# Kernel optimization log

Measured on AMD Instinct MI355X. Metric: run time of the kernel, lower is better.

Reference implementation:

```python
import jax, jax.numpy as jnp
import numpy as np

HID = 64        # HID_DIM of seq2seq encoder
NL = 2          # N_LAYERS
D = HID * NL    # dim_hidden = 128
TYPES = 16      # node op types; Input=0, Const=1
MAX_ET = 32     # max edge_type id
NUM_ROUNDS = 2


def _gru_cell(x, h, Wih, Whh, bih, bhh):
    # torch GRU gate ordering: r, z, n
    gi = x @ Wih.T + bih
    gh = h @ Whh.T + bhh
    ir, iz, inn = jnp.split(gi, 3, axis=-1)
    hr, hz, hn = jnp.split(gh, 3, axis=-1)
    r = jax.nn.sigmoid(ir + hr)
    z = jax.nn.sigmoid(iz + hz)
    n = jnp.tanh(inn + r * hn)
    return (1.0 - z) * n + z * h


def _posenc(n, d):
    pos = jnp.arange(n, dtype=jnp.float32)[:, None]
    i = jnp.arange(d // 2, dtype=jnp.float32)[None, :]
    inv = jnp.exp(-jnp.log(10000.0) * (2.0 * i / d))
    pe = jnp.zeros((n, d), jnp.float32)
    pe = pe.at[:, 0::2].set(jnp.sin(pos * inv))
    pe = pe.at[:, 1::2].set(jnp.cos(pos * inv))
    return pe


def _forward(x, edge_index, edge_type, sim_res, seq_len,
             enc_Wih0, enc_Whh0, enc_bih0, enc_bhh0,
             enc_Wih1, enc_Whh1, enc_bih1, enc_bhh1,
             Wq, Wk, Wv, op_emb, mlp_W1, mlp_b1, mlp_W2, mlp_b2,
             gru_Wih, gru_Whh, gru_bih, gru_bhh):
    N = x.shape[0]
    # --- seq2seq encode (2-layer GRU over time), computed for all nodes then masked ---
    xs = jnp.swapaxes(sim_res[:, :seq_len, :], 0, 1)  # [T, N, W]
    h0 = jnp.zeros((N, HID), sim_res.dtype)
    h1 = jnp.zeros((N, HID), sim_res.dtype)

    def step(carry, xt):
        h0, h1 = carry
        h0 = _gru_cell(xt, h0, enc_Wih0, enc_Whh0, enc_bih0, enc_bhh0)
        h1 = _gru_cell(h0, h1, enc_Wih1, enc_Whh1, enc_bih1, enc_bhh1)
        return (h0, h1), None

    (h0, h1), _ = jax.lax.scan(step, (h0, h1), xs)
    enc = jnp.concatenate([h0, h1], axis=-1)  # [N, D] = permute(1,0,2).flatten(1)
    mask = (x[:, 0] == 1) | (x[:, 1] == 1)    # Input | Const nodes
    node_emb = jnp.where(mask[:, None], enc, 0.0)

    src, dst = edge_index[0], edge_index[1]
    edge_op = jnp.argmax(x[dst], axis=1)       # [E]
    pe = _posenc(MAX_ET, D)
    edge_feat = pe[edge_type] + op_emb[edge_op]  # [E, D]
    scale = 1.0 / jnp.sqrt(jnp.float32(D))

    for _ in range(NUM_ROUNDS):
        kf = node_emb[src] + edge_feat         # [E, D]
        q = node_emb[dst] @ Wq.T
        k = kf @ Wk.T
        v = kf @ Wv.T
        score = jnp.sum(q * k, axis=-1) * scale  # [E]
        m = jax.ops.segment_max(score, dst, num_segments=N)
        ex = jnp.exp(score - m[dst])
        den = jax.ops.segment_sum(ex, dst, num_segments=N)
        alpha = ex / (den[dst] + 1e-9)
        aggr = jax.ops.segment_sum(alpha[:, None] * v, dst, num_segments=N)  # [N, D]
        aggr = jax.nn.relu(aggr @ mlp_W1.T + mlp_b1) @ mlp_W2.T + mlp_b2
        node_emb = _gru_cell(aggr, node_emb, gru_Wih, gru_Whh, gru_bih, gru_bhh)
    return node_emb


def setup_inputs() -> dict:
    key = jax.random.key(0)
    ks = jax.random.split(key, 24)
    N, E, T, W = 20000, 320000, 32, 32
    s = 0.05

    def g(k, shape):
        return jax.random.normal(k, shape, dtype=jnp.float32) * s

    node_type = jax.random.randint(ks[0], (N,), 0, TYPES)
    x = jax.nn.one_hot(node_type, TYPES, dtype=jnp.float32)
    edge_index = jax.random.randint(ks[1], (2, E), 0, N)
    edge_type = jax.random.randint(ks[2], (E,), 0, MAX_ET)
    sim_res = jax.random.uniform(ks[3], (N, T, W), dtype=jnp.float32)
    return {
        "x": x, "edge_index": edge_index, "edge_type": edge_type,
        "sim_res": sim_res, "seq_len": 32,
        "enc_Wih0": g(ks[4], (3 * HID, W)), "enc_Whh0": g(ks[5], (3 * HID, HID)),
        "enc_bih0": g(ks[6], (3 * HID,)), "enc_bhh0": g(ks[7], (3 * HID,)),
        "enc_Wih1": g(ks[8], (3 * HID, HID)), "enc_Whh1": g(ks[9], (3 * HID, HID)),
        "enc_bih1": g(ks[10], (3 * HID,)), "enc_bhh1": g(ks[11], (3 * HID,)),
        "Wq": g(ks[12], (D, D)), "Wk": g(ks[13], (D, D)), "Wv": g(ks[14], (D, D)),
        "op_emb": g(ks[15], (TYPES, D)),
        "mlp_W1": g(ks[16], (D, D)), "mlp_b1": g(ks[17], (D,)),
        "mlp_W2": g(ks[18], (D, D)), "mlp_b2": g(ks[19], (D,)),
        "gru_Wih": g(ks[20], (3 * D, D)), "gru_Whh": g(ks[21], (3 * D, D)),
        "gru_bih": g(ks[22], (3 * D,)), "gru_bhh": g(ks[23], (3 * D,)),
    }


def reference(x, edge_index, edge_type, sim_res, seq_len,
              enc_Wih0, enc_Whh0, enc_bih0, enc_bhh0,
              enc_Wih1, enc_Whh1, enc_bih1, enc_bhh1,
              Wq, Wk, Wv, op_emb, mlp_W1, mlp_b1, mlp_W2, mlp_b2,
              gru_Wih, gru_Whh, gru_bih, gru_bhh):
    return _forward(x, edge_index, edge_type, sim_res, seq_len,
                    enc_Wih0, enc_Whh0, enc_bih0, enc_bhh0,
                    enc_Wih1, enc_Whh1, enc_bih1, enc_bhh1,
                    Wq, Wk, Wv, op_emb, mlp_W1, mlp_b1, mlp_W2, mlp_b2,
                    gru_Wih, gru_Whh, gru_bih, gru_bhh)
```

## Files before the change

### kernel.cpp

```cpp
#include <hip/hip_runtime.h>

typedef unsigned int uint;
typedef unsigned short ushort;

typedef __attribute__((ext_vector_type(8))) short bf8;
typedef __attribute__((ext_vector_type(4))) float f32x4;
typedef _Float16 half_t;
typedef __attribute__((ext_vector_type(8))) half_t h8;

__device__ __forceinline__ ushort f2bf(float f){
  uint u = __builtin_bit_cast(uint, f);
  u = u + 0x7FFFu + ((u >> 16) & 1u);
  return (ushort)(u >> 16);
}
__device__ __forceinline__ float bfl(uint u){ return __builtin_bit_cast(float, u << 16); }
__device__ __forceinline__ float bfh(uint u){ return __builtin_bit_cast(float, u & 0xFFFF0000u); }
__device__ __forceinline__ uint pkhalf(float a, float b){
  ushort lo = __builtin_bit_cast(ushort, (half_t)a);
  ushort hi = __builtin_bit_cast(ushort, (half_t)b);
  return (uint)lo | ((uint)hi << 16);
}
__device__ __forceinline__ float sigmoidf_(float x){ return 1.0f/(1.0f + __expf(-x)); }
__device__ __forceinline__ float tanhf_(float x){
  x = fminf(15.0f, fmaxf(-15.0f, x));
  float t = __expf(-2.0f*x);
  return (1.0f - t)/(1.0f + t);
}
__device__ __forceinline__ f32x4 mfma_f16(h8 a, h8 b, f32x4 c){
  return __builtin_amdgcn_mfma_f32_16x16x32_f16(a, b, c, 0, 0, 0);
}
__device__ __forceinline__ f32x4 mfma_bf(bf8 a, bf8 b, f32x4 c){
  return __builtin_amdgcn_mfma_f32_16x16x32_bf16(a, b, c, 0, 0, 0);
}
__device__ __forceinline__ h8 ldw8(const float* p){
  f32x4 a = *(const f32x4*)p, b = *(const f32x4*)(p+4);
  h8 v;
  #pragma unroll
  for (int j=0;j<4;j++){ v[j] = (half_t)a[j]; v[4+j] = (half_t)b[j]; }
  return v;
}

__global__ __launch_bounds__(256) void k_prep(const float* __restrict__ x,
    const int* __restrict__ dst,
    int* __restrict__ typ, int* __restrict__ mlist, int* __restrict__ cnt,
    int* __restrict__ deg, float* __restrict__ Hf, ushort* __restrict__ Hb,
    int N, int E){
  int i = blockIdx.x*256 + threadIdx.x;
  int total = gridDim.x*256;
  if (i < N){
    const float* xr = x + (size_t)i*16;
    int t = 0;
    #pragma unroll
    for (int j=0;j<16;j++) if (xr[j] > 0.5f) t = j;
    typ[i] = t;
    if (t < 2){
      int p = atomicAdd(cnt, 1);
      mlist[p] = i;
    }
  }
  if (i < E) atomicAdd(&deg[dst[i]], 1);
  f32x4 z4 = (f32x4)0.0f;
  for (int j = i; j < N*32; j += total) ((f32x4*)Hf)[j] = z4;
  uint2 z2; z2.x = 0u; z2.y = 0u;
  for (int j = i; j < N*32; j += total) ((uint2*)Hb)[j] = z2;
}

__global__ __launch_bounds__(256) void k_cvt(
    const float* wq, const float* wk, const float* wv,
    const float* w1, const float* w2, const float* wih, const float* whh,
    const float* __restrict__ op_emb,
    ushort* oqkv, ushort* o1, ushort* o2, ushort* oih, ushort* ohh,
    ushort* __restrict__ EF){
  int i = blockIdx.x*256 + threadIdx.x;
  int stride = gridDim.x*256;
  for (int j=i; j<16384; j+=stride){
    oqkv[j]       = f2bf(wq[j]);
    oqkv[16384+j] = f2bf(wk[j]);
    oqkv[32768+j] = f2bf(wv[j]);
    o1[j] = f2bf(w1[j]);
    o2[j] = f2bf(w2[j]);
  }
  for (int j=i; j<49152; j+=stride){ oih[j]=f2bf(wih[j]); ohh[j]=f2bf(whh[j]); }
  for (int idx=i; idx<512*128; idx+=stride){
    int r = idx >> 7, d = idx & 127;
    int et = r >> 4, op = r & 15;
    int j = d >> 1;
    float inv = __expf(-0.1439115683f * (float)j);
    float ang = (float)et * inv;
    float v = (d & 1) ? __cosf(ang) : __sinf(ang);
    EF[idx] = f2bf(v + op_emb[op*128 + d]);
  }
}

template<int RELU, int HASBIAS>
__global__ __launch_bounds__(256) void k_gemm(
    const ushort* __restrict__ A, const ushort* __restrict__ B,
    const float* __restrict__ bias, ushort* __restrict__ C, int M, int N){
  int lane = threadIdx.x & 63, wv = threadIdx.x >> 6;
  int tM = blockIdx.x*64 + (wv>>1)*32;
  int tN = blockIdx.y*64 + (wv&1)*32;
  int r16 = lane & 15, kg = (lane>>4)*8;
  f32x4 acc[2][2];
  #pragma unroll
  for (int i=0;i<2;i++)
    #pragma unroll
    for (int j=0;j<2;j++) acc[i][j] = (f32x4)0.0f;
  #pragma unroll
  for (int k0=0;k0<128;k0+=32){
    bf8 a[2], b[2];
    #pragma unroll
    for (int i=0;i<2;i++){
      int row = tM + i*16 + r16; if (row > M-1) row = M-1;
      a[i] = *(const bf8*)(A + (size_t)row*128 + k0 + kg);
    }
    #pragma unroll
    for (int j=0;j<2;j++){
      int col = tN + j*16 + r16;
      b[j] = *(const bf8*)(B + (size_t)col*128 + k0 + kg);
    }
    #pragma unroll
    for (int i=0;i<2;i++)
      #pragma unroll
      for (int j=0;j<2;j++)
        acc[i][j] = __builtin_amdgcn_mfma_f32_16x16x32_bf16(a[i], b[j], acc[i][j], 0, 0, 0);
  }
  #pragma unroll
  for (int i=0;i<2;i++)
    #pragma unroll
    for (int j=0;j<2;j++){
      int col = tN + j*16 + r16;
      float bs = HASBIAS ? bias[col] : 0.0f;
      #pragma unroll
      for (int q=0;q<4;q++){
        int row = tM + i*16 + (lane>>4)*4 + q;
        if (row < M){
          float v = acc[i][j][q] + bs;
          if (RELU) v = fmaxf(v, 0.0f);
          C[(size_t)row*N + col] = f2bf(v);
        }
      }
    }
}

__global__ __launch_bounds__(512, 1) void k_enc4(
    const float* __restrict__ sim_res, const int* __restrict__ seqlen,
    const float* __restrict__ Wih0, const float* __restrict__ Whh0,
    const float* __restrict__ bih0, const float* __restrict__ bhh0,
    const float* __restrict__ Wih1, const float* __restrict__ Whh1,
    const float* __restrict__ bih1, const float* __restrict__ bhh1,
    const int* __restrict__ mlist, const int* __restrict__ cntp,
    float* __restrict__ Hf, ushort* __restrict__ Hb){
  int C = *cntp;
  int base = blockIdx.x * 16;
  if (C == 0 || base >= C) return;
  int tid = threadIdx.x;
  int w = tid >> 6, l = tid & 63;
  int node = l & 15, hi = l >> 4;
  int grp = w >> 2;
  int ws  = w & 3;

  __shared__ int nod[16];
  __shared__ __align__(16) float  Xs[16*32*32];
  __shared__ __align__(16) ushort H0h[2][16*64], H1h[2][16*64];

  if (tid < 16){
    int idx = base + tid;
    nod[tid] = mlist[idx < C ? idx : C-1];
  }
  for (int i = tid; i < 16*64; i += 512){
    H0h[0][i] = 0; H0h[1][i] = 0; H1h[0][i] = 0; H1h[1][i] = 0;
  }
  __syncthreads();

  for (int m = tid; m < 4096; m += 512){
    int nm = m >> 8, tt = (m >> 3) & 31, c = m & 7;
    int cs = c ^ (nm & 7);
    f32x4 v = *(const f32x4*)(sim_res + (size_t)nod[nm]*1024 + tt*32 + cs*4);
    *(f32x4*)(Xs + m*4) = v;
  }

  int rr = 16*ws + node;
  h8 zf;
  #pragma unroll
  for (int j=0;j<8;j++) zf[j] = (half_t)0.f;
  h8 Ai_r[2] = {zf, zf}, Ai_z[2] = {zf, zf}, Ai_n[2] = {zf, zf};
  h8 Ah_r[2], Ah_z[2], Ah_n[2];
  if (grp == 0){
    Ai_r[0] = ldw8(Wih0 + (size_t)rr*32        + hi*8);
    Ai_z[0] = ldw8(Wih0 + (size_t)(64+rr)*32   + hi*8);
    Ai_n[0] = ldw8(Wih0 + (size_t)(128+rr)*32  + hi*8);
    #pragma unroll
    for (int s=0;s<2;s++){
      Ah_r[s] = ldw8(Whh0 + (size_t)rr*64       + s*32 + hi*8);
      Ah_z[s] = ldw8(Whh0 + (size_t)(64+rr)*64  + s*32 + hi*8);
      Ah_n[s] = ldw8(Whh0 + (size_t)(128+rr)*64 + s*32 + hi*8);
    }
  } else {
    #pragma unroll
    for (int s=0;s<2;s++){
      Ai_r[s] = ldw8(Wih1 + (size_t)rr*64       + s*32 + hi*8);
      Ai_z[s] = ldw8(Wih1 + (size_t)(64+rr)*64  + s*32 + hi*8);
      Ai_n[s] = ldw8(Wih1 + (size_t)(128+rr)*64 + s*32 + hi*8);
      Ah_r[s] = ldw8(Whh1 + (size_t)rr*64       + s*32 + hi*8);
      Ah_z[s] = ldw8(Whh1 + (size_t)(64+rr)*64  + s*32 + hi*8);
      Ah_n[s] = ldw8(Whh1 + (size_t)(128+rr)*64 + s*32 + hi*8);
    }
  }
  const float* bi = grp ? bih1 : bih0;
  const float* bh = grp ? bhh1 : bhh0;
  float br[4], bz[4], bni[4], bnh[4];
  #pragma unroll
  for (int q=0;q<4;q++){
    int row = 16*ws + hi*4 + q;
    br[q]  = bi[row]      + bh[row];
    bz[q]  = bi[64+row]   + bh[64+row];
    bni[q] = bi[128+row];
    bnh[q] = bh[128+row];
  }

  int T = *seqlen; if (T > 32) T = 32; if (T < 0) T = 0;
  float hm[4] = {0.f, 0.f, 0.f, 0.f};

  const int swz = (node & 7) << 4;
  const int wo  = node * 128;
  const int wba = 32*ws + 8*hi;
  const int rd0 = wo + ((16*hi) ^ swz);
  const int rd1 = wo + ((64 + 16*hi) ^ swz);
  const int xc0 = (2*hi)   ^ (node & 7);
  const int xc1 = (2*hi+1) ^ (node & 7);
  const float* xrow = Xs + node*1024;

  __syncthreads();

  for (int k = 0; k <= T; ++k){
    int cur = k & 1;
    bool act = grp ? (k >= 1) : (k < T);
    if (act){
      h8 in0 = zf, in1 = zf, st0, st1;
      if (grp == 0){
        f32x4 xa = *(const f32x4*)(xrow + k*32 + xc0*4);
        f32x4 xb = *(const f32x4*)(xrow + k*32 + xc1*4);
        #pragma unroll
        for (int j=0;j<4;j++){ in0[j] = (half_t)xa[j]; in0[4+j] = (half_t)xb[j]; }
        st0 = *(const h8*)((const char*)H0h[cur] + rd0);
        st1 = *(const h8*)((const char*)H0h[cur] + rd1);
      } else {
        in0 = *(const h8*)((const char*)H0h[cur] + rd0);
        in1 = *(const h8*)((const char*)H0h[cur] + rd1);
        st0 = *(const h8*)((const char*)H1h[cur] + rd0);
        st1 = *(const h8*)((const char*)H1h[cur] + rd1);
      }
      f32x4 ar = {br[0],br[1],br[2],br[3]};
      f32x4 az = {bz[0],bz[1],bz[2],bz[3]};
      f32x4 an = {bni[0],bni[1],bni[2],bni[3]};
      f32x4 hn = {bnh[0],bnh[1],bnh[2],bnh[3]};
      ar = mfma_f16(Ai_r[0], in0, ar);
      az = mfma_f16(Ai_z[0], in0, az);
      an = mfma_f16(Ai_n[0], in0, an);
      if (grp){
        ar = mfma_f16(Ai_r[1], in1, ar);
        az = mfma_f16(Ai_z[1], in1, az);
        an = mfma_f16(Ai_n[1], in1, an);
      }
      ar = mfma_f16(Ah_r[0], st0, ar); ar = mfma_f16(Ah_r[1], st1, ar);
      az = mfma_f16(Ah_z[0], st0, az); az = mfma_f16(Ah_z[1], st1, az);
      hn = mfma_f16(Ah_n[0], st0, hn); hn = mfma_f16(Ah_n[1], st1, hn);
      #pragma unroll
      for (int q=0;q<4;q++){
        float r = sigmoidf_(ar[q]);
        float z = sigmoidf_(az[q]);
        float n = tanhf_(an[q] + r*hn[q]);
        hm[q] = (1.f - z)*n + z*hm[q];
      }
      char* outb = grp ? (char*)H1h[cur^1] : (char*)H0h[cur^1];
      *(uint*)(outb + wo + ( wba      ^ swz)) = pkhalf(hm[0], hm[1]);
      *(uint*)(outb + wo + ((wba + 4) ^ swz)) = pkhalf(hm[2], hm[3]);
    }
    __syncthreads();
  }

  if (base + node < C){
    int nd = nod[node];
    int off = grp ? 64 : 0;
    #pragma unroll
    for (int q=0;q<4;q++){
      int j = off + 16*ws + hi*4 + q;
      Hf[(size_t)nd*128 + j] = hm[q];
      Hb[(size_t)nd*128 + j] = f2bf(hm[q]);
    }
  }
}

__global__ __launch_bounds__(1024) void k_scan(const int* __restrict__ deg,
    int* __restrict__ rowptr, int* __restrict__ cursor, int N){
  __shared__ int wsum[16];
  __shared__ int carry_s;
  int tid = threadIdx.x, lane = tid & 63, wid = tid >> 6;
  if (tid == 0) carry_s = 0;
  __syncthreads();
  int nch = (N + 1023) / 1024;
  for (int c=0; c<nch; ++c){
    int i = c*1024 + tid;
    int v = (i < N) ? deg[i] : 0;
    int x = v;
    #pragma unroll
    for (int off=1; off<64; off<<=1){
      int t = __shfl_up(x, off, 64);
      if (lane >= off) x += t;
    }
    if (lane == 63) wsum[wid] = x;
    __syncthreads();
    int base = carry_s;
    int woff = 0;
    for (int w2=0; w2<wid; ++w2) woff += wsum[w2];
    int excl = base + woff + x - v;
    if (i < N){ rowptr[i] = excl; cursor[i] = excl; }
    __syncthreads();
    if (tid == 0){
      int s = 0;
      for (int w2=0; w2<16; ++w2) s += wsum[w2];
      carry_s = base + s;
    }
    __syncthreads();
  }
  if (tid == 0) rowptr[N] = carry_s;
}

__global__ __launch_bounds__(256) void k_scatter(const int* __restrict__ src,
    const int* __restrict__ dst, const int* __restrict__ etype, const int* __restrict__ typ,
    int* __restrict__ cursor, int* __restrict__ es_src, int* __restrict__ es_tab, int E){
  int e = blockIdx.x*256 + threadIdx.x;
  if (e < E){
    int d = dst[e];
    int pos = atomicAdd(&cursor[d], 1);
    es_src[pos] = src[e];
    es_tab[pos] = etype[e]*16 + typ[d];
  }
}

__global__ __launch_bounds__(256) void k_attn(
    const uint* __restrict__ QKV, const uint* __restrict__ KVT,
    const int* __restrict__ rowptr, const int* __restrict__ es_src, const int* __restrict__ es_tab,
    uint* __restrict__ aggr, int N){
  int w = threadIdx.x >> 6, lane = threadIdx.x & 63;
  int dst = blockIdx.x*4 + w;
  if (dst >= N) return;
  uint qu = QKV[(size_t)dst*192 + lane];
  const float scale = 0.08838834764831845f;
  float q0 = bfl(qu)*scale, q1 = bfh(qu)*scale;
  int s0 = rowptr[dst], s1 = rowptr[dst+1];
  float m = -1e30f, den = 0.f, a0 = 0.f, a1 = 0.f;
  int p = s0;
  for (; p + 4 <= s1; p += 4){
    int se[4], te[4];
    #pragma unroll
    for (int e=0;e<4;e++){ se[e] = es_src[p+e]; te[e] = es_tab[p+e]; }
    uint ku[4], kt[4], vu[4], vt[4];
    #pragma unroll
    for (int e=0;e<4;e++){
      ku[e] = QKV[(size_t)se[e]*192 + 64 + lane];
      kt[e] = KVT[(size_t)te[e]*128 + lane];
      vu[e] = QKV[(size_t)se[e]*192 + 128 + lane];
      vt[e] = KVT[(size_t)te[e]*128 + 64 + lane];
    }
    float s[4];
    #pragma unroll
    for (int e=0;e<4;e++)
      s[e] = q0*(bfl(ku[e])+bfl(kt[e])) + q1*(bfh(ku[e])+bfh(kt[e]));
    #pragma unroll
    for (int off=32; off; off>>=1){
      #pragma unroll
      for (int e=0;e<4;e++) s[e] += __shfl_xor(s[e], off);
    }
    float nm = fmaxf(fmaxf(m, fmaxf(s[0], s[1])), fmaxf(s[2], s[3]));
    float c  = __expf(m - nm);
    float pw[4];
    #pragma unroll
    for (int e=0;e<4;e++) pw[e] = __expf(s[e] - nm);
    den = den*c + pw[0] + pw[1] + pw[2] + pw[3];
    a0 = a0*c; a1 = a1*c;
    #pragma unroll
    for (int e=0;e<4;e++){
      a0 += pw[e]*(bfl(vu[e])+bfl(vt[e]));
      a1 += pw[e]*(bfh(vu[e])+bfh(vt[e]));
    }
    m = nm;
  }
  for (; p < s1; ++p){
    int src = es_src[p], tb = es_tab[p];
    uint ku = QKV[(size_t)src*192 + 64 + lane],  kt = KVT[(size_t)tb*128 + lane];
    uint vu = QKV[(size_t)src*192 + 128 + lane], vt = KVT[(size_t)tb*128 + 64 + lane];
    float s = q0*(bfl(ku)+bfl(kt)) + q1*(bfh(ku)+bfh(kt));
    #pragma unroll
    for (int off=32; off; off>>=1) s += __shfl_xor(s, off);
    float nm = fmaxf(m, s);
    float c  = __expf(m - nm);
    float pw = __expf(s - nm);
    den = den*c + pw;
    a0  = a0*c + pw*(bfl(vu)+bfl(vt));
    a1  = a1*c + pw*(bfh(vu)+bfh(vt));
    m = nm;
  }
  float inv = 1.0f/(den + 1e-9f);
  a0 *= inv; a1 *= inv;
  aggr[(size_t)dst*64 + lane] = ((uint)f2bf(a1) << 16) | (uint)f2bf(a0);
}

__global__ __launch_bounds__(512, 2) void k_fused(
    const ushort* __restrict__ Ag,
    const ushort* __restrict__ W1b, const float* __restrict__ b1,
    const ushort* __restrict__ W2b, const float* __restrict__ b2,
    const ushort* __restrict__ Wih, const ushort* __restrict__ Whh,
    const float* __restrict__ bih, const float* __restrict__ bhh,
    const ushort* Hbf, const float* Hf_in,
    float* Hf_out, ushort* Hb_out, int M){
  int lane = threadIdx.x & 63, w = threadIdx.x >> 6;
  int nb = blockIdx.x * 32;
  int r16 = lane & 15, kq = lane >> 4;
  const int col = w*16 + r16;

  __shared__ __align__(16) ushort T[32*128];

  bf8 agld[2][4], ahld[2][4];
  #pragma unroll
  for (int i=0;i<2;i++){
    int grow = nb + i*16 + r16; if (grow > M-1) grow = M-1;
    #pragma unroll
    for (int ks=0;ks<4;ks++){
      agld[i][ks] = *(const bf8*)(Ag  + (size_t)grow*128 + ks*32 + kq*8);
      ahld[i][ks] = *(const bf8*)(Hbf + (size_t)grow*128 + ks*32 + kq*8);
    }
  }
  float hprev[2][4];
  #pragma unroll
  for (int i=0;i<2;i++)
    #pragma unroll
    for (int q=0;q<4;q++){
      int node = nb + i*16 + kq*4 + q;
      hprev[i][q] = Hf_in[(size_t)(node < M ? node : M-1)*128 + col];
    }

  {
    f32x4 a0 = (f32x4)0.0f, a1v = (f32x4)0.0f;
    #pragma unroll
    for (int ks=0; ks<4; ++ks){
      bf8 wb = *(const bf8*)(W1b + (size_t)col*128 + ks*32 + kq*8);
      a0  = mfma_bf(agld[0][ks], wb, a0);
      a1v = mfma_bf(agld[1][ks], wb, a1v);
    }
    float bs = b1[col];
    #pragma unroll
    for (int q=0;q<4;q++){
      int row0 = kq*4 + q, row1 = 16 + kq*4 + q;
      *(ushort*)((char*)T + ((row0*256 + col*2) ^ ((row0&7)<<4))) = f2bf(fmaxf(a0[q]  + bs, 0.0f));
      *(ushort*)((char*)T + ((row1*256 + col*2) ^ ((row1&7)<<4))) = f2bf(fmaxf(a1v[q] + bs, 0.0f));
    }
  }
  __syncthreads();

  {
    f32x4 a0 = (f32x4)0.0f, a1v = (f32x4)0.0f;
    #pragma unroll
    for (int ks=0; ks<4; ++ks){
      bf8 wb = *(const bf8*)(W2b + (size_t)col*128 + ks*32 + kq*8);
      bf8 ax0, ax1;
      {
        int row = r16;
        ax0 = *(const bf8*)((const char*)T + row*256 + ((ks*64 + kq*16) ^ ((row&7)<<4)));
      }
      {
        int row = 16 + r16;
        ax1 = *(const bf8*)((const char*)T + row*256 + ((ks*64 + kq*16) ^ ((row&7)<<4)));
      }
      a0  = mfma_bf(ax0, wb, a0);
      a1v = mfma_bf(ax1, wb, a1v);
    }
    __syncthreads();
    float bs = b2[col];
    #pragma unroll
    for (int q=0;q<4;q++){
      int row0 = kq*4 + q, row1 = 16 + kq*4 + q;
      *(ushort*)((char*)T + ((row0*256 + col*2) ^ ((row0&7)<<4))) = f2bf(a0[q]  + bs);
      *(ushort*)((char*)T + ((row1*256 + col*2) ^ ((row1&7)<<4))) = f2bf(a1v[q] + bs);
    }
  }
  __syncthreads();

  f32x4 ar[2], az[2], ani[2], anh[2];
  #pragma unroll
  for (int i=0;i<2;i++){
    ar[i] = (f32x4)0.0f; az[i] = (f32x4)0.0f;
    ani[i] = (f32x4)0.0f; anh[i] = (f32x4)0.0f;
  }
  #pragma unroll
  for (int ks=0; ks<4; ++ks){
    int off = ks*32 + kq*8;
    bf8 wri = *(const bf8*)(Wih + (size_t)col*128       + off);
    bf8 wrh = *(const bf8*)(Whh + (size_t)col*128       + off);
    bf8 wzi = *(const bf8*)(Wih + (size_t)(128+col)*128 + off);
    bf8 wzh = *(const bf8*)(Whh + (size_t)(128+col)*128 + off);
    bf8 wni = *(const bf8*)(Wih + (size_t)(256+col)*128 + off);
    bf8 wnh = *(const bf8*)(Whh + (size_t)(256+col)*128 + off);
    bf8 ax0, ax1;
    {
      int row = r16;
      ax0 = *(const bf8*)((const char*)T + row*256 + ((ks*64 + kq*16) ^ ((row&7)<<4)));
    }
    {
      int row = 16 + r16;
      ax1 = *(const bf8*)((const char*)T + row*256 + ((ks*64 + kq*16) ^ ((row&7)<<4)));
    }
    ar[0]  = mfma_bf(ax0,         wri, ar[0]);
    ar[0]  = mfma_bf(ahld[0][ks], wrh, ar[0]);
    az[0]  = mfma_bf(ax0,         wzi, az[0]);
    az[0]  = mfma_bf(ahld[0][ks], wzh, az[0]);
    ani[0] = mfma_bf(ax0,         wni, ani[0]);
    anh[0] = mfma_bf(ahld[0][ks], wnh, anh[0]);
    ar[1]  = mfma_bf(ax1,         wri, ar[1]);
    ar[1]  = mfma_bf(ahld[1][ks], wrh, ar[1]);
    az[1]  = mfma_bf(ax1,         wzi, az[1]);
    az[1]  = mfma_bf(ahld[1][ks], wzh, az[1]);
    ani[1] = mfma_bf(ax1,         wni, ani[1]);
    anh[1] = mfma_bf(ahld[1][ks], wnh, anh[1]);
  }
  float br_  = bih[col]     + bhh[col];
  float bz_  = bih[128+col] + bhh[128+col];
  float bni_ = bih[256+col];
  float bnh_ = bhh[256+col];
  #pragma unroll
  for (int i=0;i<2;i++)
    #pragma unroll
    for (int q=0;q<4;q++){
      int node = nb + i*16 + kq*4 + q;
      if (node < M){
        float r = sigmoidf_(ar[i][q] + br_);
        float z = sigmoidf_(az[i][q] + bz_);
        float n = tanhf_(ani[i][q] + bni_ + r*(anh[i][q] + bnh_));
        float h = hprev[i][q];
        float o = (1.f - z)*n + z*h;
        Hf_out[(size_t)node*128 + col] = o;
        Hb_out[(size_t)node*128 + col] = f2bf(o);
      }
    }
}

extern "C" void kernel_launch(void* const* d_in, const int* in_sizes, int n_in,
                              void* d_out, int out_size, void* d_ws, size_t ws_size,
                              hipStream_t stream){
  const float* x       = (const float*)d_in[0];
  const int*   ei      = (const int*)d_in[1];
  const int*   etype   = (const int*)d_in[2];
  const float* sim_res = (const float*)d_in[3];
  const int*   seqlen  = (const int*)d_in[4];
  const float* eWih0 = (const float*)d_in[5];
  const float* eWhh0 = (const float*)d_in[6];
  const float* ebih0 = (const float*)d_in[7];
  const float* ebhh0 = (const float*)d_in[8];
  const float* eWih1 = (const float*)d_in[9];
  const float* eWhh1 = (const float*)d_in[10];
  const float* ebih1 = (const float*)d_in[11];
  const float* ebhh1 = (const float*)d_in[12];
  const float* Wq = (const float*)d_in[13];
  const float* Wk = (const float*)d_in[14];
  const float* Wv = (const float*)d_in[15];
  const float* op_emb = (const float*)d_in[16];
  const float* W1 = (const float*)d_in[17];
  const float* b1 = (const float*)d_in[18];
  const float* W2 = (const float*)d_in[19];
  const float* b2 = (const float*)d_in[20];
  const float* gWih = (const float*)d_in[21];
  const float* gWhh = (const float*)d_in[22];
  const float* gbih = (const float*)d_in[23];
  const float* gbhh = (const float*)d_in[24];

  const int N = in_sizes[0] / 16;
  const int E = in_sizes[2];

  char* p = (char*)d_ws;
  auto take = [&](size_t b)->void*{ void* r = (void*)p; p += (b + 255) & ~(size_t)255; return r; };

  float*  Hf    = (float*) take((size_t)N*128*4);
  ushort* Hb    = (ushort*)take((size_t)N*128*2);
  ushort* QKV   = (ushort*)take((size_t)N*384*2);
  ushort* Ag    = (ushort*)take((size_t)N*128*2);
  ushort* EF    = (ushort*)take((size_t)512*128*2);
  ushort* KVtab = (ushort*)take((size_t)512*256*2);
  ushort* wqkv  = (ushort*)take((size_t)3*16384*2);
  ushort* w1_b  = (ushort*)take((size_t)16384*2);
  ushort* w2_b  = (ushort*)take((size_t)16384*2);
  ushort* wih_b = (ushort*)take((size_t)49152*2);
  ushort* whh_b = (ushort*)take((size_t)49152*2);
  int* typ    = (int*)take((size_t)N*4);
  int* mlist  = (int*)take((size_t)N*4);
  int* cnt    = (int*)take(256);
  int* deg    = (int*)take((size_t)N*4);
  int* rowptr = (int*)take((size_t)(N+1)*4);
  int* cursor = (int*)take((size_t)N*4);
  int* es_src = (int*)take((size_t)E*4);
  int* es_tab = (int*)take((size_t)E*4);

  hipMemsetAsync(cnt, 0, 4, stream);
  hipMemsetAsync(deg, 0, (size_t)N*4, stream);

  int gE = (E + 255) / 256;
  k_prep<<<gE, 256, 0, stream>>>(x, ei + E, typ, mlist, cnt, deg, Hf, Hb, N, E);
  k_cvt<<<256, 256, 0, stream>>>(Wq, Wk, Wv, W1, W2, gWih, gWhh, op_emb,
                                 wqkv, w1_b, w2_b, wih_b, whh_b, EF);
  k_gemm<0,0><<<dim3(8,4), 256, 0, stream>>>(EF, wqkv + 16384, nullptr, KVtab, 512, 256);
  k_enc4<<<(N+15)/16, 512, 0, stream>>>(sim_res, seqlen, eWih0, eWhh0, ebih0, ebhh0,
                                        eWih1, eWhh1, ebih1, ebhh1, mlist, cnt, Hf, Hb);
  k_scan<<<1, 1024, 0, stream>>>(deg, rowptr, cursor, N);
  k_scatter<<<gE, 256, 0, stream>>>(ei, ei + E, etype, typ, cursor, es_src, es_tab, E);

  dim3 gq((N+63)/64, 6);
  for (int r=0; r<2; ++r){
    k_gemm<0,0><<<gq, 256, 0, stream>>>(Hb, wqkv, nullptr, QKV, N, 384);
    k_attn<<<(N+3)/4, 256, 0, stream>>>((const uint*)QKV, (const uint*)KVtab,
                                        rowptr, es_src, es_tab, (uint*)Ag, N);
    float* hf_out = (r == 1) ? (float*)d_out : Hf;
    k_fused<<<(N+31)/32, 512, 0, stream>>>(Ag, w1_b, b1, w2_b, b2,
                                           wih_b, whh_b, gbih, gbhh,
                                           Hb, Hf, hf_out, Hb, N);
  }
}
```

Measured before the change: 309.0 us.

## Raise MFMA wave priority, chunk-serial scan, and unroll attention edges by two

Three unrelated changes. The GRU encoder step wraps its MFMA block in s_setprio(1)/(0) so waves issuing matrix ops get scheduling priority. The single-block prefix scan becomes a one-pass chunked scan: each thread sums a contiguous chunk, the block scans those sums once, then each thread writes its own offsets, which removes the per-chunk barrier loop. The attention edge loop drops from 4 edges per iteration to 2, lowering register pressure at the cost of less memory-level parallelism per wave.

```diff
diff --git a/kernel.cpp b/kernel.cpp
--- a/kernel.cpp
+++ b/kernel.cpp
@@ -254,6 +254,7 @@
       f32x4 az = {bz[0],bz[1],bz[2],bz[3]};
       f32x4 an = {bni[0],bni[1],bni[2],bni[3]};
       f32x4 hn = {bnh[0],bnh[1],bnh[2],bnh[3]};
+      __builtin_amdgcn_s_setprio(1);
       ar = mfma_f16(Ai_r[0], in0, ar);
       az = mfma_f16(Ai_z[0], in0, az);
       an = mfma_f16(Ai_n[0], in0, an);
@@ -265,6 +266,7 @@
       ar = mfma_f16(Ah_r[0], st0, ar); ar = mfma_f16(Ah_r[1], st1, ar);
       az = mfma_f16(Ah_z[0], st0, az); az = mfma_f16(Ah_z[1], st1, az);
       hn = mfma_f16(Ah_n[0], st0, hn); hn = mfma_f16(Ah_n[1], st1, hn);
+      __builtin_amdgcn_s_setprio(0);
       #pragma unroll
       for (int q=0;q<4;q++){
         float r = sigmoidf_(ar[q]);
@@ -294,36 +296,27 @@
 __global__ __launch_bounds__(1024) void k_scan(const int* __restrict__ deg,
     int* __restrict__ rowptr, int* __restrict__ cursor, int N){
   __shared__ int wsum[16];
-  __shared__ int carry_s;
   int tid = threadIdx.x, lane = tid & 63, wid = tid >> 6;
-  if (tid == 0) carry_s = 0;
+  int CH = (N + 1023) >> 10;
+  int start = tid * CH;
+  int local = 0;
+  for (int j=0;j<CH;j++){ int i = start+j; if (i < N) local += deg[i]; }
+  int x = local;
+  #pragma unroll
+  for (int off=1; off<64; off<<=1){
+    int t = __shfl_up(x, off, 64);
+    if (lane >= off) x += t;
+  }
+  if (lane == 63) wsum[wid] = x;
   __syncthreads();
-  int nch = (N + 1023) / 1024;
-  for (int c=0; c<nch; ++c){
-    int i = c*1024 + tid;
-    int v = (i < N) ? deg[i] : 0;
-    int x = v;
-    #pragma unroll
-    for (int off=1; off<64; off<<=1){
-      int t = __shfl_up(x, off, 64);
-      if (lane >= off) x += t;
-    }
-    if (lane == 63) wsum[wid] = x;
-    __syncthreads();
-    int base = carry_s;
-    int woff = 0;
-    for (int w2=0; w2<wid; ++w2) woff += wsum[w2];
-    int excl = base + woff + x - v;
-    if (i < N){ rowptr[i] = excl; cursor[i] = excl; }
-    __syncthreads();
-    if (tid == 0){
-      int s = 0;
-      for (int w2=0; w2<16; ++w2) s += wsum[w2];
-      carry_s = base + s;
-    }
-    __syncthreads();
-  }
-  if (tid == 0) rowptr[N] = carry_s;
+  int woff = 0;
+  for (int w2=0; w2<wid; ++w2) woff += wsum[w2];
+  int run = woff + x - local;
+  for (int j=0;j<CH;j++){
+    int i = start+j;
+    if (i < N){ rowptr[i] = run; cursor[i] = run; run += deg[i]; }
+  }
+  if (tid == 1023) rowptr[N] = run;
 }
 
 __global__ __launch_bounds__(256) void k_scatter(const int* __restrict__ src,
@@ -351,39 +344,26 @@
   int s0 = rowptr[dst], s1 = rowptr[dst+1];
   float m = -1e30f, den = 0.f, a0 = 0.f, a1 = 0.f;
   int p = s0;
-  for (; p + 4 <= s1; p += 4){
-    int se[4], te[4];
-    #pragma unroll
-    for (int e=0;e<4;e++){ se[e] = es_src[p+e]; te[e] = es_tab[p+e]; }
-    uint ku[4], kt[4], vu[4], vt[4];
-    #pragma unroll
-    for (int e=0;e<4;e++){
-      ku[e] = QKV[(size_t)se[e]*192 + 64 + lane];
-      kt[e] = KVT[(size_t)te[e]*128 + lane];
-      vu[e] = QKV[(size_t)se[e]*192 + 128 + lane];
-      vt[e] = KVT[(size_t)te[e]*128 + 64 + lane];
-    }
-    float s[4];
-    #pragma unroll
-    for (int e=0;e<4;e++)
-      s[e] = q0*(bfl(ku[e])+bfl(kt[e])) + q1*(bfh(ku[e])+bfh(kt[e]));
+  for (; p + 2 <= s1; p += 2){
+    int srcA = es_src[p],   tbA = es_tab[p];
+    int srcB = es_src[p+1], tbB = es_tab[p+1];
+    uint kuA = QKV[(size_t)srcA*192 + 64 + lane],  ktA = KVT[(size_t)tbA*128 + lane];
+    uint vuA = QKV[(size_t)srcA*192 + 128 + lane], vtA = KVT[(size_t)tbA*128 + 64 + lane];
+    uint kuB = QKV[(size_t)srcB*192 + 64 + lane],  ktB = KVT[(size_t)tbB*128 + lane];
+    uint vuB = QKV[(size_t)srcB*192 + 128 + lane], vtB = KVT[(size_t)tbB*128 + 64 + lane];
+    float sA = q0*(bfl(kuA)+bfl(ktA)) + q1*(bfh(kuA)+bfh(ktA));
+    float sB = q0*(bfl(kuB)+bfl(ktB)) + q1*(bfh(kuB)+bfh(ktB));
     #pragma unroll
     for (int off=32; off; off>>=1){
-      #pragma unroll
-      for (int e=0;e<4;e++) s[e] += __shfl_xor(s[e], off);
-    }
-    float nm = fmaxf(fmaxf(m, fmaxf(s[0], s[1])), fmaxf(s[2], s[3]));
+      sA += __shfl_xor(sA, off);
+      sB += __shfl_xor(sB, off);
+    }
+    float nm = fmaxf(m, fmaxf(sA, sB));
     float c  = __expf(m - nm);
-    float pw[4];
-    #pragma unroll
-    for (int e=0;e<4;e++) pw[e] = __expf(s[e] - nm);
-    den = den*c + pw[0] + pw[1] + pw[2] + pw[3];
-    a0 = a0*c; a1 = a1*c;
-    #pragma unroll
-    for (int e=0;e<4;e++){
-      a0 += pw[e]*(bfl(vu[e])+bfl(vt[e]));
-      a1 += pw[e]*(bfh(vu[e])+bfh(vt[e]));
-    }
+    float pA = __expf(sA - nm), pB = __expf(sB - nm);
+    den = den*c + pA + pB;
+    a0  = a0*c + pA*(bfl(vuA)+bfl(vtA)) + pB*(bfl(vuB)+bfl(vtB));
+    a1  = a1*c + pA*(bfh(vuA)+bfh(vtA)) + pB*(bfh(vuB)+bfh(vtB));
     m = nm;
   }
   for (; p < s1; ++p){
```

New measurement: 330.5 us. 7.0% more time.

## Merge weight conversion into prep kernel, add MFMA priority, chunked scan

Applied to the files above, without the earlier changes.

Folds the weight and edge-feature conversion work into the prep kernel, removing one launch. Raises wave priority around the MFMA block in the encoder GRU loop so matrix work issues ahead of other waves. Rewrites the single-block prefix scan so each thread sums a contiguous chunk, which needs one block-wide pass instead of a loop with three barriers per 1024 elements. The merged kernel's grid follows the edge count, so very small graphs give fewer threads for the conversion loops.

```diff
diff --git a/kernel.cpp b/kernel.cpp
--- a/kernel.cpp
+++ b/kernel.cpp
@@ -44,6 +44,11 @@
     const int* __restrict__ dst,
     int* __restrict__ typ, int* __restrict__ mlist, int* __restrict__ cnt,
     int* __restrict__ deg, float* __restrict__ Hf, ushort* __restrict__ Hb,
+    const float* wq, const float* wk, const float* wv,
+    const float* w1, const float* w2, const float* wih, const float* whh,
+    const float* __restrict__ op_emb,
+    ushort* oqkv, ushort* o1, ushort* o2, ushort* oih, ushort* ohh,
+    ushort* __restrict__ EF,
     int N, int E){
   int i = blockIdx.x*256 + threadIdx.x;
   int total = gridDim.x*256;
@@ -63,25 +68,15 @@
   for (int j = i; j < N*32; j += total) ((f32x4*)Hf)[j] = z4;
   uint2 z2; z2.x = 0u; z2.y = 0u;
   for (int j = i; j < N*32; j += total) ((uint2*)Hb)[j] = z2;
-}
-
-__global__ __launch_bounds__(256) void k_cvt(
-    const float* wq, const float* wk, const float* wv,
-    const float* w1, const float* w2, const float* wih, const float* whh,
-    const float* __restrict__ op_emb,
-    ushort* oqkv, ushort* o1, ushort* o2, ushort* oih, ushort* ohh,
-    ushort* __restrict__ EF){
-  int i = blockIdx.x*256 + threadIdx.x;
-  int stride = gridDim.x*256;
-  for (int j=i; j<16384; j+=stride){
+  for (int j=i; j<16384; j+=total){
     oqkv[j]       = f2bf(wq[j]);
     oqkv[16384+j] = f2bf(wk[j]);
     oqkv[32768+j] = f2bf(wv[j]);
     o1[j] = f2bf(w1[j]);
     o2[j] = f2bf(w2[j]);
   }
-  for (int j=i; j<49152; j+=stride){ oih[j]=f2bf(wih[j]); ohh[j]=f2bf(whh[j]); }
-  for (int idx=i; idx<512*128; idx+=stride){
+  for (int j=i; j<49152; j+=total){ oih[j]=f2bf(wih[j]); ohh[j]=f2bf(whh[j]); }
+  for (int idx=i; idx<512*128; idx+=total){
     int r = idx >> 7, d = idx & 127;
     int et = r >> 4, op = r & 15;
     int j = d >> 1;
@@ -254,6 +249,7 @@
       f32x4 az = {bz[0],bz[1],bz[2],bz[3]};
       f32x4 an = {bni[0],bni[1],bni[2],bni[3]};
       f32x4 hn = {bnh[0],bnh[1],bnh[2],bnh[3]};
+      __builtin_amdgcn_s_setprio(1);
       ar = mfma_f16(Ai_r[0], in0, ar);
       az = mfma_f16(Ai_z[0], in0, az);
       an = mfma_f16(Ai_n[0], in0, an);
@@ -265,6 +261,7 @@
       ar = mfma_f16(Ah_r[0], st0, ar); ar = mfma_f16(Ah_r[1], st1, ar);
       az = mfma_f16(Ah_z[0], st0, az); az = mfma_f16(Ah_z[1], st1, az);
       hn = mfma_f16(Ah_n[0], st0, hn); hn = mfma_f16(Ah_n[1], st1, hn);
+      __builtin_amdgcn_s_setprio(0);
       #pragma unroll
       for (int q=0;q<4;q++){
         float r = sigmoidf_(ar[q]);
@@ -294,36 +291,27 @@
 __global__ __launch_bounds__(1024) void k_scan(const int* __restrict__ deg,
     int* __restrict__ rowptr, int* __restrict__ cursor, int N){
   __shared__ int wsum[16];
-  __shared__ int carry_s;
   int tid = threadIdx.x, lane = tid & 63, wid = tid >> 6;
-  if (tid == 0) carry_s = 0;
+  int CH = (N + 1023) >> 10;
+  int start = tid * CH;
+  int local = 0;
+  for (int j=0;j<CH;j++){ int i = start+j; if (i < N) local += deg[i]; }
+  int x = local;
+  #pragma unroll
+  for (int off=1; off<64; off<<=1){
+    int t = __shfl_up(x, off, 64);
+    if (lane >= off) x += t;
+  }
+  if (lane == 63) wsum[wid] = x;
   __syncthreads();
-  int nch = (N + 1023) / 1024;
-  for (int c=0; c<nch; ++c){
-    int i = c*1024 + tid;
-    int v = (i < N) ? deg[i] : 0;
-    int x = v;
-    #pragma unroll
-    for (int off=1; off<64; off<<=1){
-      int t = __shfl_up(x, off, 64);
-      if (lane >= off) x += t;
-    }
-    if (lane == 63) wsum[wid] = x;
-    __syncthreads();
-    int base = carry_s;
-    int woff = 0;
-    for (int w2=0; w2<wid; ++w2) woff += wsum[w2];
-    int excl = base + woff + x - v;
-    if (i < N){ rowptr[i] = excl; cursor[i] = excl; }
-    __syncthreads();
-    if (tid == 0){
-      int s = 0;
-      for (int w2=0; w2<16; ++w2) s += wsum[w2];
-      carry_s = base + s;
-    }
-    __syncthreads();
-  }
-  if (tid == 0) rowptr[N] = carry_s;
+  int woff = 0;
+  for (int w2=0; w2<wid; ++w2) woff += wsum[w2];
+  int run = woff + x - local;
+  for (int j=0;j<CH;j++){
+    int i = start+j;
+    if (i < N){ rowptr[i] = run; cursor[i] = run; run += deg[i]; }
+  }
+  if (tid == 1023) rowptr[N] = run;
 }
 
 __global__ __launch_bounds__(256) void k_scatter(const int* __restrict__ src,
@@ -603,9 +591,9 @@
   hipMemsetAsync(deg, 0, (size_t)N*4, stream);
 
   int gE = (E + 255) / 256;
-  k_prep<<<gE, 256, 0, stream>>>(x, ei + E, typ, mlist, cnt, deg, Hf, Hb, N, E);
-  k_cvt<<<256, 256, 0, stream>>>(Wq, Wk, Wv, W1, W2, gWih, gWhh, op_emb,
-                                 wqkv, w1_b, w2_b, wih_b, whh_b, EF);
+  k_prep<<<gE, 256, 0, stream>>>(x, ei + E, typ, mlist, cnt, deg, Hf, Hb,
+                                 Wq, Wk, Wv, W1, W2, gWih, gWhh, op_emb,
+                                 wqkv, w1_b, w2_b, wih_b, whh_b, EF, N, E);
   k_gemm<0,0><<<dim3(8,4), 256, 0, stream>>>(EF, wqkv + 16384, nullptr, KVtab, 512, 256);
   k_enc4<<<(N+15)/16, 512, 0, stream>>>(sim_res, seqlen, eWih0, eWhh0, ebih0, ebhh0,
                                         eWih1, eWhh1, ebih1, ebhh1, mlist, cnt, Hf, Hb);
```

Result: slower. 317.3 us (+2.7%).
